# Kernel optimization log

Hardware: AMD Instinct MI355X
Metric: run time of the kernel (lower is better)

Reference implementation:

```python
import jax, jax.numpy as jnp
import numpy as np

M = 2          # n_mix
D_K = 128      # feature dim
TEMP = float(np.sqrt(D_K))  # temperature = d_k ** 0.5


def setup_inputs() -> dict:
    key = jax.random.key(0)
    k1, k2, k3, k4 = jax.random.split(key, 4)
    BS, N, N2 = 8, 2048, 2048
    qt = jax.random.normal(k1, (BS, N, D_K), jnp.float32)
    kt = jax.random.normal(k2, (BS, N2, D_K), jnp.float32)
    vt = jax.random.normal(k3, (BS, N2, D_K), jnp.float32)
    std = M ** -0.5
    kernel = jax.random.uniform(k4, (M, D_K), jnp.float32, -std, std)
    return {"qt": qt, "kt": kt, "vt": vt, "kernel": kernel}


def reference(qt, kt, vt, kernel):
    # channels_last path of MixtureOfSoftMaxACF.call, training=False (dropout = identity)
    BS, N, dk = qt.shape
    N2 = kt.shape[1]
    d = dk // M
    # mixture prior: softmax(kernel @ mean_q^T) over axis=1 (faithful to Softmax(axis=1))
    bar_qt = jnp.mean(qt, axis=1)                       # (BS, dk)
    prior_mix = jax.nn.softmax(kernel @ bar_qt.T, axis=1)  # (m, BS)
    prior_mix = prior_mix.reshape(BS * M, 1, 1)            # row-major reshape, as in TF
    # split features into mixtures via row-major reshape (as tf.reshape does)
    q = qt.reshape(BS * M, N, d)
    k = kt.reshape(BS * M, N2, d)
    att = jnp.einsum('bnd,bmd->bnm', q, k) / TEMP        # (BS*m, N, N2)
    att = jax.nn.softmax(att, axis=2)
    att = (att * prior_mix).reshape(BS, M, N, N2).sum(axis=1)  # (BS, N, N2)
    return att @ vt                                      # (BS, N, d_v)
```

## Files before the change

### kernel.cpp

```cpp
#include <hip/hip_runtime.h>
#include <hip/hip_fp16.h>

typedef float    f32x4 __attribute__((ext_vector_type(4)));
typedef _Float16 f16x2 __attribute__((ext_vector_type(2)));
typedef _Float16 f16x4 __attribute__((ext_vector_type(4)));
typedef _Float16 f16x8 __attribute__((ext_vector_type(8)));

#define BS 8
#define NN 2048
#define DK 128
#define DM 64
#define MIXOFF (1024 * DK)
#define QSCALE 0.12751744116926208f

#define MFMA32(a, b, c) __builtin_amdgcn_mfma_f32_16x16x32_f16((a), (b), (c), 0, 0, 0)
#define EXP2(x) __builtin_amdgcn_exp2f(x)

__device__ __forceinline__ f16x2 pkrtz(float x, float y) {
  return __builtin_bit_cast(f16x2, __builtin_amdgcn_cvt_pkrtz(x, y));
}

__device__ __forceinline__ void load_lds16(const _Float16* g, _Float16* l) {
  __builtin_amdgcn_global_load_lds(
      (const __attribute__((address_space(1))) void*)(uintptr_t)g,
      (__attribute__((address_space(3))) void*)(uint32_t)(uintptr_t)l, 16, 0, 0);
}

__global__ void prep_k(const float* __restrict__ kt, _Float16* __restrict__ kh,
                       const float* __restrict__ vt, _Float16* __restrict__ vT,
                       const float* __restrict__ qt, float* __restrict__ qpart) {
  __shared__ float tile[64][65];
  __shared__ float red[256];
  int blk = blockIdx.x;
  int t = threadIdx.x;
  if (blk < 512) {
    size_t base = (size_t)blk * 4096;
#pragma unroll
    for (int j = 0; j < 4; ++j) {
      size_t i = base + j * 1024 + t * 4;
      f32x4 v = *(const f32x4*)(kt + i);
      f16x4 h;
      h[0] = (_Float16)v[0]; h[1] = (_Float16)v[1];
      h[2] = (_Float16)v[2]; h[3] = (_Float16)v[3];
      *(f16x4*)(kh + i) = h;
    }
  } else if (blk < 1024) {
    int i2 = blk - 512;
    int b = i2 >> 6;
    int rem = i2 & 63;
    int j0 = (rem & 31) * 64;
    int c0 = (rem >> 5) * 64;
    int tx = t & 63, ty = t >> 6;
    const float* src = vt + ((size_t)b * NN + j0) * DK + c0;
#pragma unroll
    for (int rr = 0; rr < 16; ++rr) {
      int row = ty * 16 + rr;
      tile[row][tx] = src[(size_t)row * DK + tx];
    }
    __syncthreads();
    _Float16* dst = vT + ((size_t)b * DK + c0) * NN + j0;
    int chl = t >> 4;
    int k4 = (t & 15) * 4;
#pragma unroll
    for (int r2 = 0; r2 < 4; ++r2) {
      int ch = r2 * 16 + chl;
      f16x4 h;
      h[0] = (_Float16)tile[k4 + 0][ch]; h[1] = (_Float16)tile[k4 + 1][ch];
      h[2] = (_Float16)tile[k4 + 2][ch]; h[3] = (_Float16)tile[k4 + 3][ch];
      *(f16x4*)(dst + (size_t)ch * NN + k4) = h;
    }
  } else {
    int i = blk - 1024;
    int b = i >> 3, seg = i & 7;
    int c = t & 127, h = t >> 7;
    const float* p = qt + ((size_t)b * NN + seg * 256 + h * 128) * DK + c;
    float s = 0.f;
#pragma unroll 8
    for (int n = 0; n < 128; ++n) s += p[(size_t)n * DK];
    red[t] = s;
    __syncthreads();
    if (t < 128) qpart[(size_t)i * 128 + t] = red[t] + red[t + 128];
  }
}

#define STAGE(BUF, S) do {                                                \
    _Float16* db_ = stg + (BUF) * 16384;                                  \
    load_lds16(khg + gKst + (S) * 2048, db_ + t * 8);                     \
    load_lds16(vTg + gVst + (S) * 32, db_ + 4096 + t * 8);                \
    load_lds16(khg + gKst + 65536 + (S) * 2048, db_ + 8192 + t * 8);      \
    load_lds16(vTg + gVst + 1024 + (S) * 32, db_ + 12288 + t * 8);        \
  } while (0)

__global__ __launch_bounds__(512, 2) void attn_k(const float* __restrict__ qt,
                                                 const _Float16* __restrict__ khg,
                                                 const _Float16* __restrict__ vTg,
                                                 const float* __restrict__ kern,
                                                 const float* __restrict__ qpart,
                                                 float* __restrict__ out) {
  __shared__ __align__(16) char smem[65536];
  _Float16* stg = (_Float16*)smem;
  const int b = blockIdx.x & 7;
  const int qb = blockIdx.x >> 3;
  const int t = threadIdx.x;
  const int wv = t >> 6;
  const int m = wv >> 2;
  const int kh = (wv >> 1) & 1;
  const int u = wv & 1;
  const int lane = t & 63;
  const int quad = lane >> 4, l16 = lane & 15;
  const int perm = ((l16 >> 2) << 3) | (l16 & 3);
  const int bq = b * (NN * DK);
  const int bV = b * (DK * NN);

  f16x8 qf[2][2];
#pragma unroll
  for (int su = 0; su < 2; ++su)
#pragma unroll
    for (int c = 0; c < 2; ++c) {
      const float* qp_ = qt + bq + m * MIXOFF +
                         (qb * 64 + u * 32 + su * 16 + l16) * DM + quad * 8 + c * 32;
      f32x4 v0 = *(const f32x4*)qp_;
      f32x4 v1 = *(const f32x4*)(qp_ + 4);
      union { f16x8 v; f16x2 h[4]; } w;
      w.h[0] = pkrtz(v0[0] * QSCALE, v0[1] * QSCALE);
      w.h[1] = pkrtz(v0[2] * QSCALE, v0[3] * QSCALE);
      w.h[2] = pkrtz(v1[0] * QSCALE, v1[1] * QSCALE);
      w.h[3] = pkrtz(v1[2] * QSCALE, v1[3] * QSCALE);
      qf[su][c] = w.v;
    }

  const int mixu = t >> 8;
  const int qq8 = t & 255;
  const int rK = qq8 >> 3;
  const int uuK = (qq8 & 7) ^ ((rK & 3) ^ ((rK >> 3) << 1));
  const int chV = t >> 2;
  const int uuV = (t & 3) ^ ((chV + (chV >> 2)) & 3);
  const int gKst = bq + mixu * MIXOFF + rK * 64 + uuK * 8;
  const int gVst = bV + chV * NN + uuV * 8;

  const int gK = (l16 & 3) ^ ((l16 >> 2) << 1);
  const int hV = (l16 + (l16 >> 2)) & 3;
  const int kA = (quad ^ gK) * 8;
  const int kB = ((quad + 4) ^ gK) * 8;
  const int kr0 = m * 2048 + perm * 64;
  const int kr1 = m * 2048 + (perm + 4) * 64;
  const int vbase = 4096 + l16 * 32 + (quad ^ hV) * 8;
  const int khoff = kh * 8192;

  const f32x4 z = {0.f, 0.f, 0.f, 0.f};
  f32x4 acc[2][8];
  float lsum[2] = {0.f, 0.f};
#pragma unroll
  for (int su = 0; su < 2; ++su)
#pragma unroll
    for (int cc = 0; cc < 8; ++cc) acc[su][cc] = z;

  STAGE(0, 0);
  int buf = 0;
  for (int s = 0; s < 32; ++s) {
    __syncthreads();
    if (s + 1 < 32) STAGE(buf ^ 1, s + 1);
    const _Float16* sb_ = stg + buf * 16384 + khoff;
    f16x8 kf0 = *(const f16x8*)(sb_ + kr0 + kA);
    f16x8 kf1 = *(const f16x8*)(sb_ + kr0 + kB);
    f16x8 kf2 = *(const f16x8*)(sb_ + kr1 + kA);
    f16x8 kf3 = *(const f16x8*)(sb_ + kr1 + kB);
    f16x8 vf[8];
#pragma unroll
    for (int cc = 0; cc < 8; ++cc) vf[cc] = *(const f16x8*)(sb_ + vbase + cc * 512);
#pragma unroll
    for (int su = 0; su < 2; ++su) {
      f32x4 s0 = MFMA32(kf1, qf[su][1], MFMA32(kf0, qf[su][0], z));
      f32x4 s1 = MFMA32(kf3, qf[su][1], MFMA32(kf2, qf[su][0], z));
      float e0 = EXP2(s0[0]), e1 = EXP2(s0[1]), e2 = EXP2(s0[2]), e3 = EXP2(s0[3]);
      float e4 = EXP2(s1[0]), e5 = EXP2(s1[1]), e6 = EXP2(s1[2]), e7 = EXP2(s1[3]);
      lsum[su] += ((e0 + e1) + (e2 + e3)) + ((e4 + e5) + (e6 + e7));
      union { f16x8 v; f16x2 h[4]; } w;
      w.h[0] = pkrtz(e0, e1); w.h[1] = pkrtz(e2, e3);
      w.h[2] = pkrtz(e4, e5); w.h[3] = pkrtz(e6, e7);
#pragma unroll
      for (int cc = 0; cc < 8; ++cc) acc[su][cc] = MFMA32(vf[cc], w.v, acc[su][cc]);
    }
    buf ^= 1;
  }
  __syncthreads();

  float* obuf = (float*)smem;
  float* barL = (float*)(smem + 33792);
  float* lgp = (float*)(smem + 37888);
  float* exq = (float*)(smem + 37952);
  float* prp = (float*)(smem + 38016);
  float* lbuf = (float*)(smem + 38144);

#pragma unroll
  for (int su = 0; su < 2; ++su) {
    lsum[su] += __shfl_xor(lsum[su], 16);
    lsum[su] += __shfl_xor(lsum[su], 32);
  }
  for (int e = t; e < 1024; e += 512) {
    int bb = e >> 7, c = e & 127;
    float ss = 0.f;
#pragma unroll
    for (int seg = 0; seg < 8; ++seg) ss += qpart[(size_t)(bb * 8 + seg) * 128 + c];
    barL[e] = ss * (1.0f / 2048.0f);
  }
  if (kh == 0 && quad == 0)
#pragma unroll
    for (int su = 0; su < 2; ++su) lbuf[m * 64 + u * 32 + su * 16 + l16] = lsum[su];
  __syncthreads();
  if (kh == 1 && quad == 0)
#pragma unroll
    for (int su = 0; su < 2; ++su) lbuf[m * 64 + u * 32 + su * 16 + l16] += lsum[su];
  if (t < 16) {
    int mm = t >> 3, bb = t & 7;
    float ss = 0.f;
    for (int c = 0; c < DK; ++c) ss += kern[mm * DK + c] * barL[bb * 128 + c];
    lgp[t] = ss;
  }
  __syncthreads();
  if (t < 16) {
    int mm = t >> 3;
    float mx = lgp[mm * 8];
    for (int i = 1; i < 8; ++i) mx = fmaxf(mx, lgp[mm * 8 + i]);
    exq[t] = __expf(lgp[t] - mx);
  }
  __syncthreads();
  if (t < 16) {
    int mm = t >> 3;
    float sm = 0.f;
    for (int i = 0; i < 8; ++i) sm += exq[mm * 8 + i];
    prp[t] = exq[t] / sm;
  }
  __syncthreads();

  const float wm = prp[b * 2 + m];
  float rr[2];
#pragma unroll
  for (int su = 0; su < 2; ++su)
    rr[su] = wm / lbuf[m * 64 + u * 32 + su * 16 + l16];

  if (m == 0 && kh == 0) {
#pragma unroll
    for (int su = 0; su < 2; ++su) {
      int r_ = (u * 32 + su * 16 + l16) * 132 + quad * 4;
#pragma unroll
      for (int cc = 0; cc < 8; ++cc) *(f32x4*)&obuf[r_ + cc * 16] = acc[su][cc];
    }
  }
  __syncthreads();
  if (m == 0 && kh == 1) {
#pragma unroll
    for (int su = 0; su < 2; ++su) {
      int r_ = (u * 32 + su * 16 + l16) * 132 + quad * 4;
#pragma unroll
      for (int cc = 0; cc < 8; ++cc) {
        f32x4 o = *(const f32x4*)&obuf[r_ + cc * 16];
#pragma unroll
        for (int e = 0; e < 4; ++e) o[e] = (o[e] + acc[su][cc][e]) * rr[su];
        *(f32x4*)&obuf[r_ + cc * 16] = o;
      }
    }
  }
  __syncthreads();
  if (m == 1 && kh == 0) {
#pragma unroll
    for (int su = 0; su < 2; ++su) {
      int r_ = (u * 32 + su * 16 + l16) * 132 + quad * 4;
#pragma unroll
      for (int cc = 0; cc < 8; ++cc) {
        f32x4 o = *(const f32x4*)&obuf[r_ + cc * 16];
#pragma unroll
        for (int e = 0; e < 4; ++e) o[e] += acc[su][cc][e] * rr[su];
        *(f32x4*)&obuf[r_ + cc * 16] = o;
      }
    }
  }
  __syncthreads();
  if (m == 1 && kh == 1) {
#pragma unroll
    for (int su = 0; su < 2; ++su) {
      int r_ = (u * 32 + su * 16 + l16) * 132 + quad * 4;
#pragma unroll
      for (int cc = 0; cc < 8; ++cc) {
        f32x4 o = *(const f32x4*)&obuf[r_ + cc * 16];
#pragma unroll
        for (int e = 0; e < 4; ++e) o[e] += acc[su][cc][e] * rr[su];
        *(f32x4*)&obuf[r_ + cc * 16] = o;
      }
    }
  }
  __syncthreads();
  const int row = t >> 3;
  const int cb = (t & 7) * 16;
  float* op = out + ((size_t)b * NN + qb * 64 + row) * DK + cb;
#pragma unroll
  for (int g = 0; g < 4; ++g)
    *(f32x4*)(op + g * 4) = *(const f32x4*)&obuf[row * 132 + cb + g * 4];
}

extern "C" void kernel_launch(void* const* d_in, const int* in_sizes, int n_in,
                              void* d_out, int out_size, void* d_ws, size_t ws_size,
                              hipStream_t stream) {
  const float* qt = (const float*)d_in[0];
  const float* kt = (const float*)d_in[1];
  const float* vt = (const float*)d_in[2];
  const float* kern = (const float*)d_in[3];
  float* out = (float*)d_out;

  char* ws = (char*)d_ws;
  float* qpart = (float*)(ws + 4096);
  _Float16* khp = (_Float16*)(ws + 65536);
  _Float16* vTp = khp + (size_t)BS * NN * DK;

  prep_k<<<dim3(1088), dim3(256), 0, stream>>>(kt, khp, vt, vTp, qt, qpart);
  attn_k<<<dim3(256), dim3(512), 0, stream>>>(qt, khp, vTp, kern, qpart, out);
}
```

Measured before the change: 115.5 us.

## Load V fragments directly from global into registers, double-buffered across unrolled steps

V tiles no longer go through LDS via global_load_lds; each wave now loads its V fragments straight from global memory into registers using an inline-asm dwordx4 load. The main loop is unrolled by two with ping-pong register buffers, so the next step's V loads overlap the current step's MFMAs. LDS staging shrinks to K only, cutting shared memory from 64KB to 40KB. In exchange, several waves redundantly fetch the same V data, which raises L2/global traffic. The inline asm load also relies on the barrier's implicit waitcnt for correctness.

```diff
diff --git a/kernel.cpp b/kernel.cpp
--- a/kernel.cpp
+++ b/kernel.cpp
@@ -24,6 +24,12 @@
   __builtin_amdgcn_global_load_lds(
       (const __attribute__((address_space(1))) void*)(uintptr_t)g,
       (__attribute__((address_space(3))) void*)(uint32_t)(uintptr_t)l, 16, 0, 0);
+}
+
+__device__ __forceinline__ f16x8 gload16v(const _Float16* p) {
+  f16x8 r;
+  asm volatile("global_load_dwordx4 %0, %1, off" : "=v"(r) : "v"(p));
+  return r;
 }
 
 __global__ void prep_k(const float* __restrict__ kt, _Float16* __restrict__ kh,
@@ -84,11 +90,37 @@
 }
 
 #define STAGE(BUF, S) do {                                                \
-    _Float16* db_ = stg + (BUF) * 16384;                                  \
+    _Float16* db_ = stg + (BUF) * 8192;                                   \
     load_lds16(khg + gKst + (S) * 2048, db_ + t * 8);                     \
-    load_lds16(vTg + gVst + (S) * 32, db_ + 4096 + t * 8);                \
-    load_lds16(khg + gKst + 65536 + (S) * 2048, db_ + 8192 + t * 8);      \
-    load_lds16(vTg + gVst + 1024 + (S) * 32, db_ + 12288 + t * 8);        \
+    load_lds16(khg + gKst + 65536 + (S) * 2048, db_ + 4096 + t * 8);      \
+  } while (0)
+
+#define VLOAD(VF, S) do {                                                 \
+    _Pragma("unroll")                                                     \
+    for (int cc = 0; cc < 8; ++cc)                                        \
+      VF[cc] = gload16v(vp0 + (size_t)(cc * 16) * NN + (S) * 32);         \
+  } while (0)
+
+#define CSTEP(BUF, VF) do {                                               \
+    const _Float16* sb_ = stg + (BUF) * 8192 + khoff;                     \
+    f16x8 kf0 = *(const f16x8*)(sb_ + kr0 + kA);                          \
+    f16x8 kf1 = *(const f16x8*)(sb_ + kr0 + kB);                          \
+    f16x8 kf2 = *(const f16x8*)(sb_ + kr1 + kA);                          \
+    f16x8 kf3 = *(const f16x8*)(sb_ + kr1 + kB);                          \
+    _Pragma("unroll")                                                     \
+    for (int su = 0; su < 2; ++su) {                                      \
+      f32x4 s0 = MFMA32(kf1, qf[su][1], MFMA32(kf0, qf[su][0], z));       \
+      f32x4 s1 = MFMA32(kf3, qf[su][1], MFMA32(kf2, qf[su][0], z));       \
+      float e0 = EXP2(s0[0]), e1 = EXP2(s0[1]), e2 = EXP2(s0[2]), e3 = EXP2(s0[3]); \
+      float e4 = EXP2(s1[0]), e5 = EXP2(s1[1]), e6 = EXP2(s1[2]), e7 = EXP2(s1[3]); \
+      lsum[su] += ((e0 + e1) + (e2 + e3)) + ((e4 + e5) + (e6 + e7));      \
+      union { f16x8 v; f16x2 h[4]; } w;                                   \
+      w.h[0] = pkrtz(e0, e1); w.h[1] = pkrtz(e2, e3);                     \
+      w.h[2] = pkrtz(e4, e5); w.h[3] = pkrtz(e6, e7);                     \
+      _Pragma("unroll")                                                   \
+      for (int cc = 0; cc < 8; ++cc)                                      \
+        acc[su][cc] = MFMA32(VF[cc], w.v, acc[su][cc]);                   \
+    }                                                                     \
   } while (0)
 
 __global__ __launch_bounds__(512, 2) void attn_k(const float* __restrict__ qt,
@@ -97,7 +129,7 @@
                                                  const float* __restrict__ kern,
                                                  const float* __restrict__ qpart,
                                                  float* __restrict__ out) {
-  __shared__ __align__(16) char smem[65536];
+  __shared__ __align__(16) char smem[40960];
   _Float16* stg = (_Float16*)smem;
   const int b = blockIdx.x & 7;
   const int qb = blockIdx.x >> 3;
@@ -133,19 +165,16 @@
   const int qq8 = t & 255;
   const int rK = qq8 >> 3;
   const int uuK = (qq8 & 7) ^ ((rK & 3) ^ ((rK >> 3) << 1));
-  const int chV = t >> 2;
-  const int uuV = (t & 3) ^ ((chV + (chV >> 2)) & 3);
   const int gKst = bq + mixu * MIXOFF + rK * 64 + uuK * 8;
-  const int gVst = bV + chV * NN + uuV * 8;
 
   const int gK = (l16 & 3) ^ ((l16 >> 2) << 1);
-  const int hV = (l16 + (l16 >> 2)) & 3;
   const int kA = (quad ^ gK) * 8;
   const int kB = ((quad + 4) ^ gK) * 8;
   const int kr0 = m * 2048 + perm * 64;
   const int kr1 = m * 2048 + (perm + 4) * 64;
-  const int vbase = 4096 + l16 * 32 + (quad ^ hV) * 8;
-  const int khoff = kh * 8192;
+  const int khoff = kh * 4096;
+
+  const _Float16* vp0 = vTg + bV + (size_t)l16 * NN + kh * 1024 + quad * 8;
 
   const f32x4 z = {0.f, 0.f, 0.f, 0.f};
   f32x4 acc[2][8];
@@ -155,33 +184,18 @@
 #pragma unroll
     for (int cc = 0; cc < 8; ++cc) acc[su][cc] = z;
 
+  f16x8 va[8], vb[8];
   STAGE(0, 0);
-  int buf = 0;
-  for (int s = 0; s < 32; ++s) {
+  VLOAD(va, 0);
+  for (int s = 0; s < 32; s += 2) {
     __syncthreads();
-    if (s + 1 < 32) STAGE(buf ^ 1, s + 1);
-    const _Float16* sb_ = stg + buf * 16384 + khoff;
-    f16x8 kf0 = *(const f16x8*)(sb_ + kr0 + kA);
-    f16x8 kf1 = *(const f16x8*)(sb_ + kr0 + kB);
-    f16x8 kf2 = *(const f16x8*)(sb_ + kr1 + kA);
-    f16x8 kf3 = *(const f16x8*)(sb_ + kr1 + kB);
-    f16x8 vf[8];
-#pragma unroll
-    for (int cc = 0; cc < 8; ++cc) vf[cc] = *(const f16x8*)(sb_ + vbase + cc * 512);
-#pragma unroll
-    for (int su = 0; su < 2; ++su) {
-      f32x4 s0 = MFMA32(kf1, qf[su][1], MFMA32(kf0, qf[su][0], z));
-      f32x4 s1 = MFMA32(kf3, qf[su][1], MFMA32(kf2, qf[su][0], z));
-      float e0 = EXP2(s0[0]), e1 = EXP2(s0[1]), e2 = EXP2(s0[2]), e3 = EXP2(s0[3]);
-      float e4 = EXP2(s1[0]), e5 = EXP2(s1[1]), e6 = EXP2(s1[2]), e7 = EXP2(s1[3]);
-      lsum[su] += ((e0 + e1) + (e2 + e3)) + ((e4 + e5) + (e6 + e7));
-      union { f16x8 v; f16x2 h[4]; } w;
-      w.h[0] = pkrtz(e0, e1); w.h[1] = pkrtz(e2, e3);
-      w.h[2] = pkrtz(e4, e5); w.h[3] = pkrtz(e6, e7);
-#pragma unroll
-      for (int cc = 0; cc < 8; ++cc) acc[su][cc] = MFMA32(vf[cc], w.v, acc[su][cc]);
-    }
-    buf ^= 1;
+    STAGE(1, s + 1);
+    VLOAD(vb, s + 1);
+    CSTEP(0, va);
+    __syncthreads();
+    if (s + 2 < 32) STAGE(0, s + 2);
+    VLOAD(va, (s + 2) & 31);
+    CSTEP(1, vb);
   }
   __syncthreads();
 
```

Measured after the change: 160.0 us. 1.39x slower.
